# Optimization experiments

Measured on AMD Instinct MI355X. Metric: run time of the kernel, lower is better.

Reference implementation:

```python
import jax, jax.numpy as jnp
import numpy as np

N, E = 50000, 800000
D_IN_N, D_IN_E, D_OUT = 64, 64, 64


def setup_inputs() -> dict:
    key = jax.random.key(0)
    ks = jax.random.split(key, 10)
    stdv = 1.0 / np.sqrt(D_OUT)
    u = lambda k, shape: jax.random.uniform(k, shape, jnp.float32, -stdv, stdv)
    return {
        "nf": jax.random.normal(ks[0], (N, D_IN_N), jnp.float32),
        "ef": jax.random.normal(ks[1], (E, D_IN_E), jnp.float32),
        "src": jax.random.randint(ks[2], (E,), 0, N, jnp.int32),
        "dst": jax.random.randint(ks[3], (E,), 0, N, jnp.int32),
        "W_node": u(ks[4], (D_IN_N, D_OUT)),
        "W_edge": u(ks[5], (D_IN_E, D_OUT)),
        "bias_node": u(ks[6], (D_OUT,)),
        "bias_edge": u(ks[7], (D_OUT,)),
        "W_dense": u(ks[8], (2 * D_OUT, D_OUT)),  # Linear(2*out, out) weight, stored transposed
        "b_dense": u(ks[9], (D_OUT,)),
    }


def reference(nf, ef, src, dst, W_node, W_edge, bias_node, bias_edge, W_dense, b_dense):
    n_nodes = nf.shape[0]
    # input projections
    nf_h = nf @ W_node                     # [N, D]
    ef_h = ef @ W_edge                     # [E, D]
    # update_all: mean of incoming edge features per dst node (0 for isolated nodes, DGL default)
    deg = jax.ops.segment_sum(jnp.ones((ef_h.shape[0],), ef_h.dtype), dst, num_segments=n_nodes)
    nb_ef = jax.ops.segment_sum(ef_h, dst, num_segments=n_nodes) / jnp.maximum(deg, 1.0)[:, None]
    # apply_nodes: nf = act(nf + bias)
    nf_out = jax.nn.relu(nf_h + bias_node)
    # apply_edges (uses updated nf): cat([ef + nb_ef[dst], (nf[src]+nf[dst])/2]) -> Linear -> +bias -> act
    tmp_ef = ef_h + nb_ef[dst]             # [E, D]
    srcdst_nf = (nf_out[src] + nf_out[dst]) * 0.5
    ef_out = jnp.concatenate([tmp_ef, srcdst_nf], axis=1) @ W_dense + b_dense + bias_edge
    ef_out = jax.nn.relu(ef_out)
    return nf_out, ef_out
```

## Files before the change

kernel.cpp:

```cpp
#include <hip/hip_runtime.h>

#define D 64

typedef __attribute__((ext_vector_type(8))) short short8;
typedef __attribute__((ext_vector_type(4))) float f32x4;

__device__ __forceinline__ ushort f2b(float f) {
    union { float f; unsigned u; } x; x.f = f;
    unsigned r = x.u + 0x7FFFu + ((x.u >> 16) & 1u);
    return (ushort)(r >> 16);
}
__device__ __forceinline__ float b2f(ushort u) {
    union { float f; unsigned u; } x; x.u = ((unsigned)u) << 16;
    return x.f;
}
__device__ __forceinline__ short8 pack8(float4 a, float4 b) {
    short8 r;
    r[0] = (short)f2b(a.x); r[1] = (short)f2b(a.y); r[2] = (short)f2b(a.z); r[3] = (short)f2b(a.w);
    r[4] = (short)f2b(b.x); r[5] = (short)f2b(b.y); r[6] = (short)f2b(b.z); r[7] = (short)f2b(b.w);
    return r;
}

#define LDA 72

__global__ __launch_bounds__(256) void fused_front_kernel(
    const float* __restrict__ nf, const float* __restrict__ Wn,
    const float* __restrict__ bias, const float* __restrict__ Wd,
    float* __restrict__ out, ushort* __restrict__ nfp_b, int N,
    const int* __restrict__ dst, int* __restrict__ deg_i, int E,
    const float* __restrict__ W_edge, const float* __restrict__ b_dense,
    const float* __restrict__ bias_edge, ushort* __restrict__ Wcomb_b,
    float* __restrict__ bias2, int NPB, int HB)
{
    __shared__ ushort Bn[64 * LDA];
    __shared__ ushort Bd[64 * LDA];
    __shared__ ushort Vs[64 * LDA];
    const int tid = threadIdx.x;
    const int bid = blockIdx.x;

    if (bid < NPB) {
        const long row0 = (long)bid * 64;
        const int w = tid >> 6, lane = tid & 63;
        const int lr = lane & 15, g = lane >> 4;
        const bool odd = lane & 1;

        {
            int k = tid >> 2, n0 = (tid & 3) * 16;
            const float4* wr = (const float4*)(Wn + (long)k * D + n0);
            float4 v0 = wr[0], v1 = wr[1], v2 = wr[2], v3 = wr[3];
            float vs[16] = {v0.x, v0.y, v0.z, v0.w, v1.x, v1.y, v1.z, v1.w,
                            v2.x, v2.y, v2.z, v2.w, v3.x, v3.y, v3.z, v3.w};
            #pragma unroll
            for (int j = 0; j < 16; ++j) Bn[(n0 + j) * LDA + k] = f2b(vs[j]);
            const float4* wd = (const float4*)(Wd + (long)(D + k) * D + n0);
            float4 u0 = wd[0], u1 = wd[1], u2 = wd[2], u3 = wd[3];
            float us[16] = {u0.x, u0.y, u0.z, u0.w, u1.x, u1.y, u1.z, u1.w,
                            u2.x, u2.y, u2.z, u2.w, u3.x, u3.y, u3.z, u3.w};
            #pragma unroll
            for (int j = 0; j < 16; ++j) Bd[(n0 + j) * LDA + k] = f2b(0.5f * us[j]);
        }

        long era = row0 + 16 * w + lr; if (era >= N) era = N - 1;
        const float4* ap = (const float4*)(nf + era * D);
        float4 v0 = ap[2 * g], v1 = ap[2 * g + 1];
        float4 v2 = ap[8 + 2 * g], v3 = ap[8 + 2 * g + 1];
        short8 a0 = pack8(v0, v1), a1 = pack8(v2, v3);
        __syncthreads();

        f32x4 acc[4];
        #pragma unroll
        for (int t = 0; t < 4; ++t) {
            f32x4 z = {0.f, 0.f, 0.f, 0.f};
            short8 b0 = *(const short8*)&Bn[(16 * t + lr) * LDA + 8 * g];
            short8 b1 = *(const short8*)&Bn[(16 * t + lr) * LDA + 32 + 8 * g];
            z = __builtin_amdgcn_mfma_f32_16x16x32_bf16(a0, b0, z, 0, 0, 0);
            z = __builtin_amdgcn_mfma_f32_16x16x32_bf16(a1, b1, z, 0, 0, 0);
            acc[t] = z;
        }
        #pragma unroll
        for (int t = 0; t < 4; ++t) {
            int c = 16 * t + lr;
            float bb = bias[c];
            #pragma unroll
            for (int reg = 0; reg < 4; ++reg) {
                int r = 16 * w + 4 * g + reg;
                float v = fmaxf(acc[t][reg] + bb, 0.f);
                long rg = row0 + r;
                if (rg < N) out[rg * D + c] = v;
                Vs[r * LDA + c] = f2b(v);
            }
        }
        __syncthreads();

        short8 c0 = *(const short8*)&Vs[(16 * w + lr) * LDA + 8 * g];
        short8 c1 = *(const short8*)&Vs[(16 * w + lr) * LDA + 32 + 8 * g];
        f32x4 acc2[4];
        #pragma unroll
        for (int t = 0; t < 4; ++t) {
            f32x4 z = {0.f, 0.f, 0.f, 0.f};
            short8 b0 = *(const short8*)&Bd[(16 * t + lr) * LDA + 8 * g];
            short8 b1 = *(const short8*)&Bd[(16 * t + lr) * LDA + 32 + 8 * g];
            z = __builtin_amdgcn_mfma_f32_16x16x32_bf16(c0, b0, z, 0, 0, 0);
            z = __builtin_amdgcn_mfma_f32_16x16x32_bf16(c1, b1, z, 0, 0, 0);
            acc2[t] = z;
        }
        const int rb = 16 * w + 4 * g + (odd ? 2 : 0);
        long e0 = row0 + rb, e1 = row0 + rb + 1;
        #pragma unroll
        for (int t = 0; t < 4; ++t) {
            float p0 = __shfl_xor(acc2[t][0], 1, 64);
            float p1 = __shfl_xor(acc2[t][1], 1, 64);
            float p2 = __shfl_xor(acc2[t][2], 1, 64);
            float p3 = __shfl_xor(acc2[t][3], 1, 64);
            float lo0, hi0, lo1, hi1;
            if (odd) { lo0 = p2; hi0 = acc2[t][2]; lo1 = p3; hi1 = acc2[t][3]; }
            else     { lo0 = acc2[t][0]; hi0 = p0; lo1 = acc2[t][1]; hi1 = p1; }
            int cbase = 16 * t + (lr & ~1);
            unsigned dw0 = ((unsigned)f2b(hi0) << 16) | (unsigned)f2b(lo0);
            unsigned dw1 = ((unsigned)f2b(hi1) << 16) | (unsigned)f2b(lo1);
            if (e0 < N) *(unsigned*)(nfp_b + e0 * D + cbase) = dw0;
            if (e1 < N) *(unsigned*)(nfp_b + e1 * D + cbase) = dw1;
        }
    } else if (bid < NPB + HB) {
        int i = (bid - NPB) * 256 + tid;
        if (i < E) atomicAdd(deg_i + dst[i], 1);
    } else {
        for (int idx = tid; idx < D * D; idx += 256) {
            int k = idx >> 6, n = idx & 63;
            float s = 0.f;
            #pragma unroll 8
            for (int j = 0; j < D; ++j)
                s = fmaf(W_edge[k * D + j], Wd[j * D + n], s);
            Wcomb_b[n * D + k] = f2b(s);
        }
        if (tid < D) bias2[tid] = b_dense[tid] + bias_edge[tid];
    }
}

__global__ __launch_bounds__(256) void scanA_kernel(
    const int* __restrict__ deg_i, int* __restrict__ pos,
    int* __restrict__ bsum, int N)
{
    __shared__ int s[256];
    const int tid = threadIdx.x;
    const int i = blockIdx.x * 256 + tid;
    int v = (i < N) ? deg_i[i] : 0;
    s[tid] = v;
    __syncthreads();
    #pragma unroll
    for (int off = 1; off < 256; off <<= 1) {
        int t = (tid >= off) ? s[tid - off] : 0;
        __syncthreads();
        s[tid] += t;
        __syncthreads();
    }
    if (i < N) pos[i] = s[tid] - v;
    if (tid == 255) bsum[blockIdx.x] = s[255];
}

__global__ __launch_bounds__(256) void scanB_kernel(int* __restrict__ bsum, int NB)
{
    __shared__ int s[256];
    const int tid = threadIdx.x;
    int v = (tid < NB) ? bsum[tid] : 0;
    s[tid] = v;
    __syncthreads();
    #pragma unroll
    for (int off = 1; off < 256; off <<= 1) {
        int t = (tid >= off) ? s[tid - off] : 0;
        __syncthreads();
        s[tid] += t;
        __syncthreads();
    }
    if (tid < NB) bsum[tid] = s[tid] - v;
}

__global__ __launch_bounds__(256) void scanC_kernel(
    const int* __restrict__ pos, int* __restrict__ cursor,
    const int* __restrict__ bsum, int N)
{
    int i = blockIdx.x * 256 + threadIdx.x;
    if (i < N) cursor[i] = pos[i] + bsum[blockIdx.x];
}

__global__ __launch_bounds__(256) void scatter_kernel(
    const int* __restrict__ dst, const int* __restrict__ src,
    int* __restrict__ cursor, int4* __restrict__ sorted_eds, int E)
{
    int i = blockIdx.x * 256 + threadIdx.x;
    if (i < E) {
        int dv = dst[i];
        int slot = atomicAdd(cursor + dv, 1);
        sorted_eds[slot] = make_int4(i, dv, src[i], 0);
    }
}

#define SEG_ROWS 256
#define SLSTR 34
__global__ __launch_bounds__(256) void efp_seg_kernel(
    const float* __restrict__ ef, const int4* __restrict__ sorted_eds,
    const ushort* __restrict__ Wt, ushort* __restrict__ efp,
    float* __restrict__ nb_sum, int E)
{
    __shared__ unsigned Slds[SEG_ROWS * SLSTR];
    __shared__ int dsts[SEG_ROWS];
    const int tid = threadIdx.x;
    const long s0 = (long)blockIdx.x * SEG_ROWS;

    const int w = tid >> 6, lane = tid & 63;
    const int lr = lane & 15, g = lane >> 4;
    const bool odd = lane & 1;

    long gde[4];
    #pragma unroll
    for (int tt = 0; tt < 4; ++tt) {
        long s = s0 + 64 * tt + 16 * w + lr;
        if (s >= E) s = E - 1;
        gde[tt] = (long)sorted_eds[s].x;
    }
    float4 va[4][4];
    #pragma unroll
    for (int tt = 0; tt < 4; ++tt) {
        const float4* ap = (const float4*)(ef + gde[tt] * D);
        va[tt][0] = ap[2 * g];     va[tt][1] = ap[2 * g + 1];
        va[tt][2] = ap[8 + 2 * g]; va[tt][3] = ap[8 + 2 * g + 1];
    }
    {
        long s = s0 + tid;
        dsts[tid] = (s < E) ? sorted_eds[s].y : -1;
    }

    short8 bf0[4], bf1[4];
    #pragma unroll
    for (int t = 0; t < 4; ++t) {
        bf0[t] = *(const short8*)&Wt[(16 * t + lr) * D + 8 * g];
        bf1[t] = *(const short8*)&Wt[(16 * t + lr) * D + 32 + 8 * g];
    }

    #pragma unroll
    for (int tt = 0; tt < 4; ++tt) {
        short8 a0 = pack8(va[tt][0], va[tt][1]);
        short8 a1 = pack8(va[tt][2], va[tt][3]);
        f32x4 acc[4];
        #pragma unroll
        for (int t = 0; t < 4; ++t) {
            f32x4 z = {0.f, 0.f, 0.f, 0.f};
            z = __builtin_amdgcn_mfma_f32_16x16x32_bf16(a0, bf0[t], z, 0, 0, 0);
            z = __builtin_amdgcn_mfma_f32_16x16x32_bf16(a1, bf1[t], z, 0, 0, 0);
            acc[t] = z;
        }

        const int rb = 64 * tt + 16 * w + 4 * g + (odd ? 2 : 0);
        long sl0 = s0 + rb, sl1 = s0 + rb + 1;
        #pragma unroll
        for (int t = 0; t < 4; ++t) {
            float p0 = __shfl_xor(acc[t][0], 1, 64);
            float p1 = __shfl_xor(acc[t][1], 1, 64);
            float p2 = __shfl_xor(acc[t][2], 1, 64);
            float p3 = __shfl_xor(acc[t][3], 1, 64);
            float lo0, hi0, lo1, hi1;
            if (odd) { lo0 = p2; hi0 = acc[t][2]; lo1 = p3; hi1 = acc[t][3]; }
            else     { lo0 = acc[t][0]; hi0 = p0; lo1 = acc[t][1]; hi1 = p1; }
            int cbase = 16 * t + (lr & ~1);
            int dc = cbase >> 1;
            unsigned dw0 = ((unsigned)f2b(hi0) << 16) | (unsigned)f2b(lo0);
            unsigned dw1 = ((unsigned)f2b(hi1) << 16) | (unsigned)f2b(lo1);
            if (sl0 < E) *(unsigned*)(efp + sl0 * D + cbase) = dw0;
            if (sl1 < E) *(unsigned*)(efp + sl1 * D + cbase) = dw1;
            Slds[rb * SLSTR + dc]       = dw0;
            Slds[(rb + 1) * SLSTR + dc] = dw1;
        }
    }
    __syncthreads();

    {
        const int dwc = tid & 31;
        const int r0 = (tid >> 5) * 32;
        float seg0 = 0.f, seg1 = 0.f;
        int cur = dsts[r0];
        #pragma unroll 4
        for (int r = r0; r < r0 + 32; ++r) {
            int dv = dsts[r];
            unsigned u = Slds[r * SLSTR + dwc];
            if (dv != cur) {
                if (cur >= 0) {
                    atomicAdd(nb_sum + (long)cur * D + 2 * dwc, seg0);
                    atomicAdd(nb_sum + (long)cur * D + 2 * dwc + 1, seg1);
                }
                seg0 = seg1 = 0.f;
                cur = dv;
            }
            seg0 += b2f((ushort)(u & 0xffff));
            seg1 += b2f((ushort)(u >> 16));
        }
        if (cur >= 0) {
            atomicAdd(nb_sum + (long)cur * D + 2 * dwc, seg0);
            atomicAdd(nb_sum + (long)cur * D + 2 * dwc + 1, seg1);
        }
    }
}

__global__ __launch_bounds__(256) void ndp_lite_kernel(
    const float* __restrict__ nb_sum, const int* __restrict__ deg_i,
    const ushort* __restrict__ nfp_b, ushort* __restrict__ ndp_b, int N)
{
    long i = (long)blockIdx.x * 256 + threadIdx.x;
    long node = i >> 3;
    int cb = (int)(i & 7);
    if (node >= N) return;
    float inv = 1.0f / fmaxf((float)deg_i[node], 1.0f);
    const float4* sp = (const float4*)(nb_sum + node * D + cb * 8);
    float4 x0 = sp[0], x1 = sp[1];
    short8 np = *(const short8*)(nfp_b + node * D + cb * 8);
    short8 r;
    r[0] = (short)f2b(x0.x * inv + b2f((ushort)np[0]));
    r[1] = (short)f2b(x0.y * inv + b2f((ushort)np[1]));
    r[2] = (short)f2b(x0.z * inv + b2f((ushort)np[2]));
    r[3] = (short)f2b(x0.w * inv + b2f((ushort)np[3]));
    r[4] = (short)f2b(x1.x * inv + b2f((ushort)np[4]));
    r[5] = (short)f2b(x1.y * inv + b2f((ushort)np[5]));
    r[6] = (short)f2b(x1.z * inv + b2f((ushort)np[6]));
    r[7] = (short)f2b(x1.w * inv + b2f((ushort)np[7]));
    *(short8*)(ndp_b + node * D + cb * 8) = r;
}

__global__ __launch_bounds__(256) void final_kernel(
    const ushort* __restrict__ efp, const int4* __restrict__ sorted_eds,
    const ushort* __restrict__ ndp_b, const ushort* __restrict__ nfp_b,
    const float* __restrict__ bias2, float* __restrict__ out, int E)
{
    long idx = (long)blockIdx.x * 256 + threadIdx.x;
    long s = idx >> 2;
    int q = (int)(idx & 3);
    if (s >= E) return;
    int4 ed = sorted_eds[s];
    long eid = ed.x;
    int dv = ed.y, sv = ed.z;
    const short8* ep = (const short8*)(efp + s * D + q * 16);
    const short8* np = (const short8*)(ndp_b + (long)dv * D + q * 16);
    const short8* sp = (const short8*)(nfp_b + (long)sv * D + q * 16);
    short8 e0 = ep[0], e1 = ep[1];
    short8 n0 = np[0], n1 = np[1];
    short8 s0 = sp[0], s1 = sp[1];
    const float4* bp = (const float4*)(bias2 + q * 16);
    float4 b0 = bp[0], b1 = bp[1], b2 = bp[2], b3 = bp[3];

    float r[16];
    #pragma unroll
    for (int j = 0; j < 8; ++j) {
        r[j]     = b2f((ushort)e0[j]) + b2f((ushort)n0[j]) + b2f((ushort)s0[j]);
        r[8 + j] = b2f((ushort)e1[j]) + b2f((ushort)n1[j]) + b2f((ushort)s1[j]);
    }
    float4* op = (float4*)(out + eid * D + q * 16);
    op[0] = make_float4(fmaxf(r[0] + b0.x, 0.f), fmaxf(r[1] + b0.y, 0.f),
                        fmaxf(r[2] + b0.z, 0.f), fmaxf(r[3] + b0.w, 0.f));
    op[1] = make_float4(fmaxf(r[4] + b1.x, 0.f), fmaxf(r[5] + b1.y, 0.f),
                        fmaxf(r[6] + b1.z, 0.f), fmaxf(r[7] + b1.w, 0.f));
    op[2] = make_float4(fmaxf(r[8] + b2.x, 0.f), fmaxf(r[9] + b2.y, 0.f),
                        fmaxf(r[10] + b2.z, 0.f), fmaxf(r[11] + b2.w, 0.f));
    op[3] = make_float4(fmaxf(r[12] + b3.x, 0.f), fmaxf(r[13] + b3.y, 0.f),
                        fmaxf(r[14] + b3.z, 0.f), fmaxf(r[15] + b3.w, 0.f));
}

extern "C" void kernel_launch(void* const* d_in, const int* in_sizes, int n_in,
                              void* d_out, int out_size, void* d_ws, size_t ws_size,
                              hipStream_t stream) {
    const float* nf        = (const float*)d_in[0];
    const float* ef        = (const float*)d_in[1];
    const int*   src       = (const int*)d_in[2];
    const int*   dst       = (const int*)d_in[3];
    const float* W_node    = (const float*)d_in[4];
    const float* W_edge    = (const float*)d_in[5];
    const float* bias_node = (const float*)d_in[6];
    const float* bias_edge = (const float*)d_in[7];
    const float* W_dense   = (const float*)d_in[8];
    const float* b_dense   = (const float*)d_in[9];

    const int N = in_sizes[0] / D;
    const int E = in_sizes[1] / D;
    const int NB = (N + 255) / 256;
    const int NPB = (N + 63) / 64;
    const int HB = (E + 255) / 256;

    float* nf_out = (float*)d_out;
    float* ef_out = (float*)d_out + (size_t)N * D;

    char* p = (char*)d_ws;
    int*    deg_i    = (int*)p;     p += (size_t)N * 4;
    float*  nb_sum   = (float*)p;   p += (size_t)N * D * 4;
    size_t  zbytes   = (size_t)(p - (char*)d_ws);
    int*    pos      = (int*)p;     p += (size_t)N * 4;
    int*    cursor   = (int*)p;     p += (size_t)N * 4;
    int*    bsum     = (int*)p;     p += 256 * 4;
    int4*   sorted_eds=(int4*)p;    p += (size_t)E * 16;
    ushort* nfp_b    = (ushort*)p;  p += (size_t)N * D * 2;
    ushort* ndp_b    = (ushort*)p;  p += (size_t)N * D * 2;
    ushort* Wcomb_b  = (ushort*)p;  p += D * D * 2;
    float*  bias2    = (float*)p;   p += 256;
    ushort* efp      = (ushort*)p;

    hipMemsetAsync(d_ws, 0, zbytes, stream);

    fused_front_kernel<<<NPB + HB + 1, 256, 0, stream>>>(
        nf, W_node, bias_node, W_dense, nf_out, nfp_b, N,
        dst, deg_i, E, W_edge, b_dense, bias_edge, Wcomb_b, bias2, NPB, HB);
    scanA_kernel<<<NB, 256, 0, stream>>>(deg_i, pos, bsum, N);
    scanB_kernel<<<1, 256, 0, stream>>>(bsum, NB);
    scanC_kernel<<<NB, 256, 0, stream>>>(pos, cursor, bsum, N);
    scatter_kernel<<<(E + 255) / 256, 256, 0, stream>>>(dst, src, cursor, sorted_eds, E);
    efp_seg_kernel<<<(E + SEG_ROWS - 1) / SEG_ROWS, 256, 0, stream>>>(
        ef, sorted_eds, Wcomb_b, efp, nb_sum, E);
    ndp_lite_kernel<<<(int)(((size_t)N * 8 + 255) / 256), 256, 0, stream>>>(
        nb_sum, deg_i, nfp_b, ndp_b, N);
    final_kernel<<<(int)(((size_t)E * 4 + 255) / 256), 256, 0, stream>>>(
        efp, sorted_eds, ndp_b, nfp_b, bias2, ef_out, E);
}
```

Before: 343.9 us.

## Fold scan finalize into scatter and node-mean into final kernel

Removes the scanC kernel by computing each edge's slot from the partial-scan position, the block offset and a zeroed per-node counter inside scatter. Removes the ndp_lite kernel by having the final edge kernel read the fp32 neighbor sums, degree and projected node features directly and do the mean there. This cuts two launches and the intermediate ndp buffer. In exchange, final_kernel now gathers fp32 rows per dst, twice the bytes of the old bf16 rows, plus an extra bf16 row and a degree read per edge.

After: 331.2 us, median of 2. -3.7%, faster.

```diff
diff --git a/kernel.cpp b/kernel.cpp
--- a/kernel.cpp
+++ b/kernel.cpp
@@ -175,22 +175,15 @@
     if (tid < NB) bsum[tid] = s[tid] - v;
 }
 
-__global__ __launch_bounds__(256) void scanC_kernel(
-    const int* __restrict__ pos, int* __restrict__ cursor,
-    const int* __restrict__ bsum, int N)
-{
-    int i = blockIdx.x * 256 + threadIdx.x;
-    if (i < N) cursor[i] = pos[i] + bsum[blockIdx.x];
-}
-
 __global__ __launch_bounds__(256) void scatter_kernel(
     const int* __restrict__ dst, const int* __restrict__ src,
-    int* __restrict__ cursor, int4* __restrict__ sorted_eds, int E)
+    const int* __restrict__ pos, const int* __restrict__ bsum,
+    int* __restrict__ cnt, int4* __restrict__ sorted_eds, int E)
 {
     int i = blockIdx.x * 256 + threadIdx.x;
     if (i < E) {
         int dv = dst[i];
-        int slot = atomicAdd(cursor + dv, 1);
+        int slot = pos[dv] + bsum[dv >> 8] + atomicAdd(cnt + dv, 1);
         sorted_eds[slot] = make_int4(i, dv, src[i], 0);
     }
 }
@@ -300,34 +293,11 @@
     }
 }
 
-__global__ __launch_bounds__(256) void ndp_lite_kernel(
-    const float* __restrict__ nb_sum, const int* __restrict__ deg_i,
-    const ushort* __restrict__ nfp_b, ushort* __restrict__ ndp_b, int N)
-{
-    long i = (long)blockIdx.x * 256 + threadIdx.x;
-    long node = i >> 3;
-    int cb = (int)(i & 7);
-    if (node >= N) return;
-    float inv = 1.0f / fmaxf((float)deg_i[node], 1.0f);
-    const float4* sp = (const float4*)(nb_sum + node * D + cb * 8);
-    float4 x0 = sp[0], x1 = sp[1];
-    short8 np = *(const short8*)(nfp_b + node * D + cb * 8);
-    short8 r;
-    r[0] = (short)f2b(x0.x * inv + b2f((ushort)np[0]));
-    r[1] = (short)f2b(x0.y * inv + b2f((ushort)np[1]));
-    r[2] = (short)f2b(x0.z * inv + b2f((ushort)np[2]));
-    r[3] = (short)f2b(x0.w * inv + b2f((ushort)np[3]));
-    r[4] = (short)f2b(x1.x * inv + b2f((ushort)np[4]));
-    r[5] = (short)f2b(x1.y * inv + b2f((ushort)np[5]));
-    r[6] = (short)f2b(x1.z * inv + b2f((ushort)np[6]));
-    r[7] = (short)f2b(x1.w * inv + b2f((ushort)np[7]));
-    *(short8*)(ndp_b + node * D + cb * 8) = r;
-}
-
 __global__ __launch_bounds__(256) void final_kernel(
     const ushort* __restrict__ efp, const int4* __restrict__ sorted_eds,
-    const ushort* __restrict__ ndp_b, const ushort* __restrict__ nfp_b,
-    const float* __restrict__ bias2, float* __restrict__ out, int E)
+    const float* __restrict__ nb_sum, const int* __restrict__ deg_i,
+    const ushort* __restrict__ nfp_b, const float* __restrict__ bias2,
+    float* __restrict__ out, int E)
 {
     long idx = (long)blockIdx.x * 256 + threadIdx.x;
     long s = idx >> 2;
@@ -336,20 +306,26 @@
     int4 ed = sorted_eds[s];
     long eid = ed.x;
     int dv = ed.y, sv = ed.z;
+
     const short8* ep = (const short8*)(efp + s * D + q * 16);
-    const short8* np = (const short8*)(ndp_b + (long)dv * D + q * 16);
+    const float4* nb = (const float4*)(nb_sum + (long)dv * D + q * 16);
+    const short8* nd = (const short8*)(nfp_b + (long)dv * D + q * 16);
     const short8* sp = (const short8*)(nfp_b + (long)sv * D + q * 16);
     short8 e0 = ep[0], e1 = ep[1];
-    short8 n0 = np[0], n1 = np[1];
+    float4 x0 = nb[0], x1 = nb[1], x2 = nb[2], x3 = nb[3];
+    short8 d0 = nd[0], d1 = nd[1];
     short8 s0 = sp[0], s1 = sp[1];
+    float inv = 1.0f / fmaxf((float)deg_i[dv], 1.0f);
     const float4* bp = (const float4*)(bias2 + q * 16);
     float4 b0 = bp[0], b1 = bp[1], b2 = bp[2], b3 = bp[3];
 
+    float xb[16] = {x0.x, x0.y, x0.z, x0.w, x1.x, x1.y, x1.z, x1.w,
+                    x2.x, x2.y, x2.z, x2.w, x3.x, x3.y, x3.z, x3.w};
     float r[16];
     #pragma unroll
     for (int j = 0; j < 8; ++j) {
-        r[j]     = b2f((ushort)e0[j]) + b2f((ushort)n0[j]) + b2f((ushort)s0[j]);
-        r[8 + j] = b2f((ushort)e1[j]) + b2f((ushort)n1[j]) + b2f((ushort)s1[j]);
+        r[j]     = b2f((ushort)e0[j]) + xb[j] * inv + b2f((ushort)d0[j]) + b2f((ushort)s0[j]);
+        r[8 + j] = b2f((ushort)e1[j]) + xb[8 + j] * inv + b2f((ushort)d1[j]) + b2f((ushort)s1[j]);
     }
     float4* op = (float4*)(out + eid * D + q * 16);
     op[0] = make_float4(fmaxf(r[0] + b0.x, 0.f), fmaxf(r[1] + b0.y, 0.f),
@@ -388,13 +364,12 @@
     char* p = (char*)d_ws;
     int*    deg_i    = (int*)p;     p += (size_t)N * 4;
     float*  nb_sum   = (float*)p;   p += (size_t)N * D * 4;
+    int*    cnt      = (int*)p;     p += (size_t)N * 4;
     size_t  zbytes   = (size_t)(p - (char*)d_ws);
     int*    pos      = (int*)p;     p += (size_t)N * 4;
-    int*    cursor   = (int*)p;     p += (size_t)N * 4;
     int*    bsum     = (int*)p;     p += 256 * 4;
     int4*   sorted_eds=(int4*)p;    p += (size_t)E * 16;
     ushort* nfp_b    = (ushort*)p;  p += (size_t)N * D * 2;
-    ushort* ndp_b    = (ushort*)p;  p += (size_t)N * D * 2;
     ushort* Wcomb_b  = (ushort*)p;  p += D * D * 2;
     float*  bias2    = (float*)p;   p += 256;
     ushort* efp      = (ushort*)p;
@@ -406,12 +381,10 @@
         dst, deg_i, E, W_edge, b_dense, bias_edge, Wcomb_b, bias2, NPB, HB);
     scanA_kernel<<<NB, 256, 0, stream>>>(deg_i, pos, bsum, N);
     scanB_kernel<<<1, 256, 0, stream>>>(bsum, NB);
-    scanC_kernel<<<NB, 256, 0, stream>>>(pos, cursor, bsum, N);
-    scatter_kernel<<<(E + 255) / 256, 256, 0, stream>>>(dst, src, cursor, sorted_eds, E);
+    scatter_kernel<<<(E + 255) / 256, 256, 0, stream>>>(dst, src, pos, bsum, cnt,
+                                                        sorted_eds, E);
     efp_seg_kernel<<<(E + SEG_ROWS - 1) / SEG_ROWS, 256, 0, stream>>>(
         ef, sorted_eds, Wcomb_b, efp, nb_sum, E);
-    ndp_lite_kernel<<<(int)(((size_t)N * 8 + 255) / 256), 256, 0, stream>>>(
-        nb_sum, deg_i, nfp_b, ndp_b, N);
     final_kernel<<<(int)(((size_t)E * 4 + 255) / 256), 256, 0, stream>>>(
-        efp, sorted_eds, ndp_b, nfp_b, bias2, ef_out, E);
-}
+        efp, sorted_eds, nb_sum, deg_i, nfp_b, bias2, ef_out, E);
+}
```
